# Performance work log

Measured on AMD Instinct MI355X. Metric: run time of the kernel, lower is better.

Reference implementation:

```python
import jax, jax.numpy as jnp
import numpy as np
import math

L, D, H, V, B, S, MR = 8, 768, 12, 32000, 2, 1024, 4
HD = D // H

def setup_inputs() -> dict:
    key = jax.random.key(0)
    ks = iter(jax.random.split(key, 64))
    def rn(shape, s=0.02):
        return jax.random.normal(next(ks), shape, jnp.float32) * s
    inp = {}
    inp['tokens'] = jax.random.randint(next(ks), (B, S), 0, V, jnp.int32)
    inp['tok_emb'] = rn((V, D))
    inp['pos_emb'] = rn((S, D))
    for n in ['Wq_row', 'Wk_row', 'Wv_row', 'Wq_col', 'Wo']:
        inp[n] = rn((L, D, D))
    for n in ['bq_row', 'bk_row', 'bv_row', 'bq_col', 'bo']:
        inp[n] = jnp.zeros((L, D), jnp.float32)
    inp['ln1_g'] = jnp.ones((L, D), jnp.float32); inp['ln1_b'] = jnp.zeros((L, D), jnp.float32)
    inp['ln2_g'] = jnp.ones((L, D), jnp.float32); inp['ln2_b'] = jnp.zeros((L, D), jnp.float32)
    inp['W1'] = rn((L, D, MR * D)); inp['b1'] = jnp.zeros((L, MR * D), jnp.float32)
    inp['W2'] = rn((L, MR * D, D)); inp['b2'] = jnp.zeros((L, D), jnp.float32)
    inp['Wk_sh'] = rn((D, D)); inp['bk_sh'] = jnp.zeros((D,), jnp.float32)
    inp['Wv_sh'] = rn((D, D)); inp['bv_sh'] = jnp.zeros((D,), jnp.float32)
    inp['lnf_g'] = jnp.ones((D,), jnp.float32); inp['lnf_b'] = jnp.zeros((D,), jnp.float32)
    inp['Whead'] = rn((D, V)); inp['bhead'] = jnp.zeros((V,), jnp.float32)
    return inp

def _ln(x, g, b, eps=1e-5):
    m = x.mean(-1, keepdims=True)
    v = ((x - m) ** 2).mean(-1, keepdims=True)
    return (x - m) * jax.lax.rsqrt(v + eps) * g + b

def _heads(x):
    b, s, _ = x.shape
    return x.reshape(b, s, H, HD).transpose(0, 2, 1, 3)  # [B,H,S,hd]

def _merge(x):
    b, h, s, hd = x.shape
    return x.transpose(0, 2, 1, 3).reshape(b, s, h * hd)

def _forward(tokens, tok_emb, pos_emb, Wq_row, bq_row, Wk_row, bk_row, Wv_row, bv_row,
             Wq_col, bq_col, Wo, bo, ln1_g, ln1_b, ln2_g, ln2_b, W1, b1, W2, b2,
             Wk_sh, bk_sh, Wv_sh, bv_sh, lnf_g, lnf_b, Whead, bhead):
    s_len = tokens.shape[1]
    inv = 1.0 / math.sqrt(HD)
    x = tok_emb[tokens] + pos_emb[:s_len]
    mask = jnp.triu(jnp.ones((s_len, s_len), bool), 1)
    past_k, past_v = [], []
    for i in range(L):
        h = _ln(x, ln1_g[i], ln1_b[i])
        q_row = _heads(h @ Wq_row[i] + bq_row[i])
        k_row = _heads(h @ Wk_row[i] + bk_row[i])
        v_row = _heads(h @ Wv_row[i] + bv_row[i])
        q_col = _heads(h @ Wq_col[i] + bq_col[i])
        k_col = _heads(h @ Wk_sh + bk_sh)   # shared KV projector (archived memory)
        v_col = _heads(h @ Wv_sh + bv_sh)
        ts = jnp.einsum('bhqd,bhkd->bhqk', q_row, k_row) * inv
        ts = jnp.where(mask, -jnp.inf, ts)
        if past_k:
            pk = jnp.stack(past_k, axis=3)  # [B,H,S,l,hd]
            pv = jnp.stack(past_v, axis=3)
            ms = jnp.einsum('bhsd,bhsld->bhsl', q_col, pk) * inv
            w = jax.nn.softmax(jnp.concatenate([ts, ms], axis=-1), axis=-1)
            tw, mw = w[..., :s_len], w[..., s_len:]
            ctx = (jnp.einsum('bhqk,bhkd->bhqd', tw, v_row)
                   + jnp.einsum('bhsl,bhsld->bhsd', mw, pv))
        else:
            ctx = jnp.einsum('bhqk,bhkd->bhqd', jax.nn.softmax(ts, axis=-1), v_row)
        x = x + (_merge(ctx) @ Wo[i] + bo[i])
        h2 = _ln(x, ln2_g[i], ln2_b[i])
        x = x + (jax.nn.gelu(h2 @ W1[i] + b1[i], approximate=False) @ W2[i] + b2[i])
        past_k.append(k_col)
        past_v.append(v_col)
    return _ln(x, lnf_g, lnf_b) @ Whead + bhead

def reference(tokens, tok_emb, pos_emb, Wq_row, bq_row, Wk_row, bk_row, Wv_row, bv_row,
              Wq_col, bq_col, Wo, bo, ln1_g, ln1_b, ln2_g, ln2_b, W1, b1, W2, b2,
              Wk_sh, bk_sh, Wv_sh, bv_sh, lnf_g, lnf_b, Whead, bhead):
    return _forward(tokens, tok_emb, pos_emb, Wq_row, bq_row, Wk_row, bk_row, Wv_row, bv_row,
                    Wq_col, bq_col, Wo, bo, ln1_g, ln1_b, ln2_g, ln2_b, W1, b1, W2, b2,
                    Wk_sh, bk_sh, Wv_sh, bv_sh, lnf_g, lnf_b, Whead, bhead)
```

## Files before the change

### kernel.cpp

```cpp
#include <hip/hip_runtime.h>
#include <hip/hip_bf16.h>
#include <math.h>

#define L_   8
#define D_   768
#define H_   12
#define V_   32000
#define B_   2
#define S_   1024
#define HD_  64
#define BS_  2048
#define DFF_ 3072

typedef __hip_bfloat16 bf16;
typedef __attribute__((ext_vector_type(8))) short bf16x8;
typedef __attribute__((ext_vector_type(4))) float f32x4;

#define CFUN(r) (((r) >> 1) & 3)

__device__ __forceinline__ void cp16(void* lds, const void* g) {
  __builtin_amdgcn_global_load_lds(
      (const __attribute__((address_space(1))) void*)g,
      (__attribute__((address_space(3))) void*)lds, 16, 0, 0);
}

__device__ __forceinline__ unsigned short f2bf(float v) {
  __hip_bfloat16 h = __float2bfloat16(v);
  return *reinterpret_cast<unsigned short*>(&h);
}
__device__ __forceinline__ float bf2f(unsigned short u) {
  return __uint_as_float(((unsigned)u) << 16);
}

__global__ __launch_bounds__(256) void k_embed(const int* __restrict__ tokens,
    const float* __restrict__ tok_emb, const float* __restrict__ pos_emb,
    float* __restrict__ x) {
  int idx = blockIdx.x * 256 + threadIdx.x;
  int row = idx / D_;
  int d   = idx - row * D_;
  int s   = row & (S_ - 1);
  int t   = tokens[row];
  x[idx] = tok_emb[(size_t)t * D_ + d] + pos_emb[(size_t)s * D_ + d];
}

__global__ __launch_bounds__(256) void k_ln(const float* __restrict__ x,
    const float* __restrict__ g, const float* __restrict__ b,
    bf16* __restrict__ out) {
  int row = blockIdx.x;
  const float* xr = x + (size_t)row * D_;
  int t = threadIdx.x;
  float v0 = xr[t], v1 = xr[t + 256], v2 = xr[t + 512];
  float s  = v0 + v1 + v2;
  float s2 = v0 * v0 + v1 * v1 + v2 * v2;
#pragma unroll
  for (int off = 32; off; off >>= 1) {
    s  += __shfl_down(s, off);
    s2 += __shfl_down(s2, off);
  }
  __shared__ float rs[4], rs2[4];
  __shared__ float mean_s, rstd_s;
  int wid = t >> 6;
  if ((t & 63) == 0) { rs[wid] = s; rs2[wid] = s2; }
  __syncthreads();
  if (t == 0) {
    float S1 = rs[0] + rs[1] + rs[2] + rs[3];
    float S2 = rs2[0] + rs2[1] + rs2[2] + rs2[3];
    float m  = S1 / D_;
    float var = S2 / D_ - m * m;
    mean_s = m;
    rstd_s = rsqrtf(var + 1e-5f);
  }
  __syncthreads();
  float m = mean_s, r = rstd_s;
  bf16* orow = out + (size_t)row * D_;
  orow[t]       = __float2bfloat16((v0 - m) * r * g[t]       + b[t]);
  orow[t + 256] = __float2bfloat16((v1 - m) * r * g[t + 256] + b[t + 256]);
  orow[t + 512] = __float2bfloat16((v2 - m) * r * g[t + 512] + b[t + 512]);
}

__global__ __launch_bounds__(256) void k_w2bf_t(const float* __restrict__ W,
    bf16* __restrict__ Wt, int K, int N, size_t ils, size_t ols) {
  __shared__ float t[32][33];
  const float* Wm = W + (size_t)blockIdx.z * ils;
  bf16* Wtm = Wt + (size_t)blockIdx.z * ols;
  int n0 = blockIdx.x * 32, k0 = blockIdx.y * 32;
  int tx = threadIdx.x;
  for (int i = threadIdx.y; i < 32; i += 8)
    t[i][tx] = Wm[(size_t)(k0 + i) * N + n0 + tx];
  __syncthreads();
  for (int i = threadIdx.y; i < 32; i += 8)
    Wtm[(size_t)(n0 + i) * K + k0 + tx] = __float2bfloat16(t[tx][i]);
}

__global__ __launch_bounds__(256) void k_bcat(const float* __restrict__ bq,
    const float* __restrict__ bk, const float* __restrict__ bqc,
    const float* __restrict__ bv, const float* __restrict__ bksh,
    const float* __restrict__ bvsh, float* __restrict__ b6) {
  int idx = blockIdx.x * 256 + threadIdx.x;
  if (idx >= L_ * 4608) return;
  int l = idx / 4608, c = idx - l * 4608;
  float v = (c < 768)  ? bq[l * 768 + c]
          : (c < 1536) ? bk[l * 768 + c - 768]
          : (c < 2304) ? bqc[l * 768 + c - 1536]
          : (c < 3072) ? bv[l * 768 + c - 2304]
          : (c < 3840) ? bksh[c - 3072]
                       : bvsh[c - 3840];
  b6[idx] = v;
}

__global__ __launch_bounds__(256) void k_red(float* __restrict__ x,
    const float* __restrict__ pk, const float* __restrict__ bias, int N) {
  const int i = (blockIdx.x * 256 + threadIdx.x) * 4;
  const int col = i % N;
  const size_t MN = (size_t)BS_ * N;
  float4 a  = *reinterpret_cast<const float4*>(x + i);
  float4 p0 = *reinterpret_cast<const float4*>(pk + i);
  float4 p1 = *reinterpret_cast<const float4*>(pk + MN + i);
  a.x += p0.x + p1.x + bias[col];
  a.y += p0.y + p1.y + bias[col + 1];
  a.z += p0.z + p1.z + bias[col + 2];
  a.w += p0.w + p1.w + bias[col + 3];
  *reinterpret_cast<float4*>(x + i) = a;
}

template <int BM, int EPI, int KSPL>
__global__ __launch_bounds__(256) void k_bgemm(
    const bf16* __restrict__ A, const bf16* __restrict__ Wt,
    const bf16* __restrict__ Wt2,
    const float* __restrict__ bias, const float* __restrict__ resid,
    float* __restrict__ Cf, bf16* __restrict__ Cb, bf16* __restrict__ Cb2,
    bf16* __restrict__ Cb3, int NM, int M, int N, int K) {
  constexpr int ASZ = BM * 64;
  constexpr int ALINES = BM / 64;
  constexpr int BSTRIDE = ASZ + 8192;
  constexpr int MF = BM / 32;
  __shared__ __align__(16) char smem[3 * BSTRIDE];
  const int tid = threadIdx.x;
  const int l = tid & 63, w = tid >> 6;
  const int wr = w >> 1, wc = w & 1;

  const int nwg = (int)gridDim.x;
  int id = (int)blockIdx.x;
  id = (id & 7) * (nwg >> 3) + (id >> 3);
  int sk = 0;
  if constexpr (KSPL == 2) {
    const int TT = nwg >> 1;
    sk = id / TT;
    id -= sk * TT;
  }
  const int m0 = (id % NM) * BM;
  const int n0 = (id / NM) * 128;
  const int kstart = sk * (K / KSPL);

  const int lane15 = l & 15, lg = l >> 4;

  const bf16* WB = Wt;
  int nb0 = n0;
  if constexpr (EPI == 6) {
    if (n0 >= 3072) { WB = Wt2; nb0 = n0 - 3072; }
  }

  const int r0 = tid >> 2, p0 = tid & 3;
  const char* aSrc[ALINES];
#pragma unroll
  for (int i = 0; i < ALINES; i++) {
    const int rr = i * 64 + r0;
    aSrc[i] = (const char*)(A + (size_t)(m0 + rr) * K + kstart) + ((p0 ^ CFUN(rr)) * 16);
  }
  const char* bSrc0 = (const char*)(WB + (size_t)(nb0 + r0) * K + kstart) + ((p0 ^ CFUN(r0)) * 16);
  const char* bSrc1 = (const char*)(WB + (size_t)(nb0 + 64 + r0) * K + kstart) + ((p0 ^ CFUN(64 + r0)) * 16);

  int aOff[MF], bOff[4];
#pragma unroll
  for (int mi = 0; mi < MF; mi++) {
    int r = wr * (BM / 2) + mi * 16 + lane15;
    aOff[mi] = r * 64 + ((lg ^ CFUN(r)) * 16);
  }
#pragma unroll
  for (int ni = 0; ni < 4; ni++) {
    int r = wc * 64 + ni * 16 + lane15;
    bOff[ni] = ASZ + r * 64 + ((lg ^ CFUN(r)) * 16);
  }

  f32x4 acc[MF][4];
#pragma unroll
  for (int mi = 0; mi < MF; mi++)
#pragma unroll
    for (int ni = 0; ni < 4; ni++) acc[mi][ni] = (f32x4){0.f, 0.f, 0.f, 0.f};

  auto stage = [&](int buf, int t) {
    const size_t kb = (size_t)t * 64;
    char* base = smem + buf * BSTRIDE;
#pragma unroll
    for (int i = 0; i < ALINES; i++)
      cp16(base + i * 4096 + w * 1024, aSrc[i] + kb);
    cp16(base + ASZ + w * 1024, bSrc0 + kb);
    cp16(base + ASZ + 4096 + w * 1024, bSrc1 + kb);
  };
  auto compute = [&](int buf) {
    const char* base = smem + buf * BSTRIDE;
    bf16x8 af[MF], bfr[4];
#pragma unroll
    for (int mi = 0; mi < MF; mi++) af[mi] = *(const bf16x8*)(base + aOff[mi]);
#pragma unroll
    for (int ni = 0; ni < 4; ni++) bfr[ni] = *(const bf16x8*)(base + bOff[ni]);
    __builtin_amdgcn_s_setprio(1);
#pragma unroll
    for (int mi = 0; mi < MF; mi++)
#pragma unroll
      for (int ni = 0; ni < 4; ni++)
        acc[mi][ni] = __builtin_amdgcn_mfma_f32_16x16x32_bf16(
            af[mi], bfr[ni], acc[mi][ni], 0, 0, 0);
    __builtin_amdgcn_s_setprio(0);
  };

  const int nk = (K / KSPL) >> 5;
  stage(0, 0);
  stage(1, 1);
  int buf = 0;
  for (int t = 0; t < nk; t++) {
    if (t + 1 < nk) {
      if constexpr (ALINES == 2) asm volatile("s_waitcnt vmcnt(4)" ::: "memory");
      else                       asm volatile("s_waitcnt vmcnt(3)" ::: "memory");
    } else {
      asm volatile("s_waitcnt vmcnt(0)" ::: "memory");
    }
    __builtin_amdgcn_s_barrier();
    if (t + 2 < nk) {
      int nb = buf + 2; if (nb >= 3) nb -= 3;
      stage(nb, t + 2);
    }
    compute(buf);
    buf = (buf == 2) ? 0 : buf + 1;
  }

#pragma unroll
  for (int ni = 0; ni < 4; ni++) {
    const int col = n0 + wc * 64 + ni * 16 + lane15;
    const float bv = bias[col];
#pragma unroll
    for (int mi = 0; mi < MF; mi++) {
      const int rowb = m0 + wr * (BM / 2) + mi * 16 + lg * 4;
      if constexpr (EPI == 6) {
        if (col < 2304) {
#pragma unroll
          for (int j = 0; j < 4; j++)
            Cb[(size_t)(rowb + j) * 2304 + col] = __float2bfloat16(acc[mi][ni][j] + bv);
        } else if (col < 3072) {
          ushort4 pk;
          pk.x = f2bf(acc[mi][ni][0] + bv);
          pk.y = f2bf(acc[mi][ni][1] + bv);
          pk.z = f2bf(acc[mi][ni][2] + bv);
          pk.w = f2bf(acc[mi][ni][3] + bv);
          const int bq = rowb >> 10, s = rowb & (S_ - 1);
          *reinterpret_cast<ushort4*>(
              (unsigned short*)Cb2 + ((size_t)(bq * 768 + (col - 2304))) * S_ + s) = pk;
        } else {
#pragma unroll
          for (int j = 0; j < 4; j++)
            Cb3[(size_t)(rowb + j) * 1536 + (col - 3072)] =
                __float2bfloat16(acc[mi][ni][j] + bv);
        }
      } else if constexpr (EPI == 7) {
#pragma unroll
        for (int j = 0; j < 4; j++)
          Cf[(size_t)sk * M * N + (size_t)(rowb + j) * N + col] = acc[mi][ni][j];
      } else {
#pragma unroll
        for (int j = 0; j < 4; j++) {
          const int row = rowb + j;
          float v = acc[mi][ni][j] + bv;
          if constexpr (EPI == 1) v += resid[(size_t)row * N + col];
          if constexpr (EPI == 2) {
            v = 0.5f * v * (1.0f + erff(v * 0.70710678118654752f));
            Cb[(size_t)row * N + col] = __float2bfloat16(v);
          } else if constexpr (EPI == 3) {
            Cb[(size_t)row * N + col] = __float2bfloat16(v);
          } else {
            Cf[(size_t)row * N + col] = v;
          }
        }
      }
    }
  }
}

#define HBAR() asm volatile("s_barrier" ::: "memory")
#define MFMA16(AF, BF, MB, NB)                                               \
  do {                                                                       \
    __builtin_amdgcn_s_setprio(1);                                           \
    _Pragma("unroll") for (int mi_ = 0; mi_ < 4; mi_++)                      \
      _Pragma("unroll") for (int ni_ = 0; ni_ < 2; ni_++)                    \
        _Pragma("unroll") for (int ks_ = 0; ks_ < 2; ks_++)                  \
          acc[(MB) + mi_][(NB) + ni_] =                                      \
              __builtin_amdgcn_mfma_f32_16x16x32_bf16(                       \
                  AF[mi_][ks_], BF[ni_][ks_], acc[(MB) + mi_][(NB) + ni_],   \
                  0, 0, 0);                                                  \
    __builtin_amdgcn_s_setprio(0);                                           \
  } while (0)

__global__ __launch_bounds__(512, 1) void k_head8(const bf16* __restrict__ A,
    const bf16* __restrict__ Wt, const float* __restrict__ bias,
    float* __restrict__ C) {
  __shared__ __align__(16) char smem[131072];
  const int tid = threadIdx.x;
  const int l = tid & 63, w = tid >> 6;
  const int wr = w >> 2, wc = w & 3;
  const int lane15 = l & 15, lg = l >> 4;

  int id = (int)blockIdx.x;
  id = (id & 7) * 125 + (id >> 3);
  const int m0 = (id % 8) * 256;
  const int n0 = (id / 8) * 256;

  auto issueA = [&](int tile, int hb) {
#pragma unroll
    for (int j = 0; j < 2; j++) {
      const int idx = j * 512 + tid;
      const int rl = idx >> 3, sl = idx & 7;
      const bf16* g = A + (size_t)(m0 + hb + rl) * 768 + tile * 64 +
                      ((sl ^ (rl & 7)) << 3);
      cp16(smem + (tile & 1) * 32768 + hb * 128 + (j * 512 + w * 64) * 16, g);
    }
  };
  auto issueB = [&](int tile, int hb) {
#pragma unroll
    for (int j = 0; j < 2; j++) {
      const int idx = j * 512 + tid;
      const int rl = idx >> 3, sl = idx & 7;
      const bf16* g = Wt + (size_t)(n0 + hb + rl) * 768 + tile * 64 +
                      ((sl ^ (rl & 7)) << 3);
      cp16(smem + 65536 + (tile & 1) * 32768 + hb * 128 + (j * 512 + w * 64) * 16, g);
    }
  };
  auto ldA = [&](int buf, int mi, int ks) {
    const int r = wr * 128 + mi * 16 + lane15;
    return *(const bf16x8*)(smem + buf * 32768 + r * 128 +
                            ((((ks << 2) + lg) ^ (r & 7)) << 4));
  };
  auto ldB = [&](int buf, int ni, int ks) {
    const int r = wc * 64 + ni * 16 + lane15;
    return *(const bf16x8*)(smem + 65536 + buf * 32768 + r * 128 +
                            ((((ks << 2) + lg) ^ (r & 7)) << 4));
  };

  f32x4 acc[8][4];
#pragma unroll
  for (int i = 0; i < 8; i++)
#pragma unroll
    for (int j = 0; j < 4; j++) acc[i][j] = (f32x4){0.f, 0.f, 0.f, 0.f};
  bf16x8 alo[4][2], ahi[4][2], blo[2][2], bhi[2][2];

  issueA(0, 0);  issueA(0, 128);  issueB(0, 0);  issueB(0, 128);
  issueB(1, 0);  issueA(1, 0);    issueB(1, 128);
  asm volatile("s_waitcnt vmcnt(6)" ::: "memory");
  HBAR();

  for (int it = 0; it < 5; ++it) {
    const int Tb = 2 * it + 1, Tn = 2 * it + 2;
#pragma unroll
    for (int mi = 0; mi < 4; mi++) { alo[mi][0] = ldA(0, mi, 0); alo[mi][1] = ldA(0, mi, 1); }
#pragma unroll
    for (int ni = 0; ni < 2; ni++) { blo[ni][0] = ldB(0, ni, 0); blo[ni][1] = ldB(0, ni, 1); }
    issueA(Tb, 128);
    HBAR(); MFMA16(alo, blo, 0, 0); HBAR();
#pragma unroll
    for (int ni = 0; ni < 2; ni++) { bhi[ni][0] = ldB(0, ni + 2, 0); bhi[ni][1] = ldB(0, ni + 2, 1); }
    HBAR(); MFMA16(alo, bhi, 0, 2); HBAR();
#pragma unroll
    for (int mi = 0; mi < 4; mi++) { ahi[mi][0] = ldA(0, mi + 4, 0); ahi[mi][1] = ldA(0, mi + 4, 1); }
    issueB(Tn, 0);
    HBAR(); MFMA16(ahi, bhi, 4, 2); HBAR();
    issueA(Tn, 0);
    issueB(Tn, 128);
    asm volatile("s_waitcnt vmcnt(6)" ::: "memory");
    HBAR(); MFMA16(ahi, blo, 4, 0); HBAR();
#pragma unroll
    for (int mi = 0; mi < 4; mi++) { alo[mi][0] = ldA(1, mi, 0); alo[mi][1] = ldA(1, mi, 1); }
#pragma unroll
    for (int ni = 0; ni < 2; ni++) { blo[ni][0] = ldB(1, ni, 0); blo[ni][1] = ldB(1, ni, 1); }
    issueA(Tn, 128);
    HBAR(); MFMA16(alo, blo, 0, 0); HBAR();
#pragma unroll
    for (int ni = 0; ni < 2; ni++) { bhi[ni][0] = ldB(1, ni + 2, 0); bhi[ni][1] = ldB(1, ni + 2, 1); }
    HBAR(); MFMA16(alo, bhi, 0, 2); HBAR();
#pragma unroll
    for (int mi = 0; mi < 4; mi++) { ahi[mi][0] = ldA(1, mi + 4, 0); ahi[mi][1] = ldA(1, mi + 4, 1); }
    issueB(Tn + 1, 0);
    HBAR(); MFMA16(ahi, bhi, 4, 2); HBAR();
    issueA(Tn + 1, 0);
    issueB(Tn + 1, 128);
    asm volatile("s_waitcnt vmcnt(6)" ::: "memory");
    HBAR(); MFMA16(ahi, blo, 4, 0); HBAR();
  }

  {
#pragma unroll
    for (int mi = 0; mi < 4; mi++) { alo[mi][0] = ldA(0, mi, 0); alo[mi][1] = ldA(0, mi, 1); }
#pragma unroll
    for (int ni = 0; ni < 2; ni++) { blo[ni][0] = ldB(0, ni, 0); blo[ni][1] = ldB(0, ni, 1); }
    issueA(11, 128);
    HBAR(); MFMA16(alo, blo, 0, 0); HBAR();
#pragma unroll
    for (int ni = 0; ni < 2; ni++) { bhi[ni][0] = ldB(0, ni + 2, 0); bhi[ni][1] = ldB(0, ni + 2, 1); }
    HBAR(); MFMA16(alo, bhi, 0, 2); HBAR();
#pragma unroll
    for (int mi = 0; mi < 4; mi++) { ahi[mi][0] = ldA(0, mi + 4, 0); ahi[mi][1] = ldA(0, mi + 4, 1); }
    HBAR(); MFMA16(ahi, bhi, 4, 2); HBAR();
    asm volatile("s_waitcnt vmcnt(0)" ::: "memory");
    HBAR(); MFMA16(ahi, blo, 4, 0); HBAR();
#pragma unroll
    for (int mi = 0; mi < 4; mi++) { alo[mi][0] = ldA(1, mi, 0); alo[mi][1] = ldA(1, mi, 1); }
#pragma unroll
    for (int ni = 0; ni < 2; ni++) { blo[ni][0] = ldB(1, ni, 0); blo[ni][1] = ldB(1, ni, 1); }
    MFMA16(alo, blo, 0, 0);
#pragma unroll
    for (int ni = 0; ni < 2; ni++) { bhi[ni][0] = ldB(1, ni + 2, 0); bhi[ni][1] = ldB(1, ni + 2, 1); }
    MFMA16(alo, bhi, 0, 2);
#pragma unroll
    for (int mi = 0; mi < 4; mi++) { ahi[mi][0] = ldA(1, mi + 4, 0); ahi[mi][1] = ldA(1, mi + 4, 1); }
    MFMA16(ahi, bhi, 4, 2);
    MFMA16(ahi, blo, 4, 0);
  }

#pragma unroll
  for (int ni = 0; ni < 4; ni++) {
    const int col = n0 + wc * 64 + ni * 16 + lane15;
    const float bv = bias[col];
#pragma unroll
    for (int mi = 0; mi < 8; mi++) {
      const int rowb = m0 + wr * 128 + mi * 16 + lg * 4;
#pragma unroll
      for (int j = 0; j < 4; j++)
        C[(size_t)(rowb + j) * 32000 + col] = acc[mi][ni][j] + bv;
    }
  }
}

__global__ __launch_bounds__(256) void k_attn(
    const bf16* __restrict__ qkv, const bf16* __restrict__ vT,
    const bf16* __restrict__ memkv, bf16* __restrict__ ctx, int layer) {
  const int bh = blockIdx.x;
  const int b = bh / H_, h = bh % H_;
  const int qt = (int)gridDim.y - 1 - (int)blockIdx.y;
  const int tid = threadIdx.x;
  const int w = tid >> 6, l = tid & 63;
  const int lane15 = l & 15, lg = l >> 4;
  const float inv = 0.125f;

  __shared__ char plds[4][2048];
  __shared__ float wlp[4][16][16];
  char* pl = plds[w];

  const int qrow0 = qt * 64 + w * 16;
  const size_t rowA = (size_t)(b * S_ + qrow0 + lane15);
  const bf16* qp = qkv + rowA * 2304 + h * 64 + lg * 8;
  const bf16x8 qf0 = *(const bf16x8*)(qp);
  const bf16x8 qf1 = *(const bf16x8*)(qp + 32);

  const bf16* kbase = qkv + (size_t)(b * S_) * 2304 + 768 + h * 64 + lg * 8;
  const bf16* vbase = vT + ((size_t)(b * 768 + h * 64 + lane15)) * S_;

  float mrow[4], dsum[4];
  f32x4 acc[4];
#pragma unroll
  for (int j = 0; j < 4; j++) { mrow[j] = -INFINITY; dsum[j] = 0.f; }
#pragma unroll
  for (int ni = 0; ni < 4; ni++) acc[ni] = (f32x4){0.f, 0.f, 0.f, 0.f};

  const int ntile = ((qrow0 + 15) >> 6) + 1;
  for (int kt64 = 0; kt64 < ntile; kt64++) {
    const int k0 = kt64 * 64;
    f32x4 sc[4];
#pragma unroll
    for (int kt = 0; kt < 4; kt++) {
      const bf16* kp = kbase + (size_t)(k0 + kt * 16 + lane15) * 2304;
      bf16x8 kf0 = *(const bf16x8*)(kp);
      bf16x8 kf1 = *(const bf16x8*)(kp + 32);
      f32x4 z = (f32x4){0.f, 0.f, 0.f, 0.f};
      z = __builtin_amdgcn_mfma_f32_16x16x32_bf16(qf0, kf0, z, 0, 0, 0);
      sc[kt] = __builtin_amdgcn_mfma_f32_16x16x32_bf16(qf1, kf1, z, 0, 0, 0);
    }
    float tmax[4];
#pragma unroll
    for (int j = 0; j < 4; j++) tmax[j] = -INFINITY;
#pragma unroll
    for (int kt = 0; kt < 4; kt++) {
      const int kabs = k0 + kt * 16 + lane15;
#pragma unroll
      for (int j = 0; j < 4; j++) {
        const int qabs = qrow0 + lg * 4 + j;
        float v = (kabs <= qabs) ? sc[kt][j] * inv : -INFINITY;
        sc[kt][j] = v;
        tmax[j] = fmaxf(tmax[j], v);
      }
    }
#pragma unroll
    for (int off = 1; off < 16; off <<= 1)
#pragma unroll
      for (int j = 0; j < 4; j++) tmax[j] = fmaxf(tmax[j], __shfl_xor(tmax[j], off, 16));

    float psum[4];
#pragma unroll
    for (int j = 0; j < 4; j++) {
      const float mnew = fmaxf(mrow[j], tmax[j]);
      const float alpha = __expf(mrow[j] - mnew);
      mrow[j] = mnew;
      dsum[j] *= alpha;
#pragma unroll
      for (int ni = 0; ni < 4; ni++) acc[ni][j] *= alpha;
      psum[j] = 0.f;
    }
#pragma unroll
    for (int kt = 0; kt < 4; kt++) {
      const int gsl = kt * 2 + (lane15 >> 3);
      const int ebyte = (lane15 & 7) * 2;
#pragma unroll
      for (int j = 0; j < 4; j++) {
        const float p = __expf(sc[kt][j] - mrow[j]);
        psum[j] += p;
        const int r = lg * 4 + j;
        *(unsigned short*)(pl + r * 128 + ((gsl ^ (r & 7)) << 4) + ebyte) = f2bf(p);
      }
    }
#pragma unroll
    for (int off = 1; off < 16; off <<= 1)
#pragma unroll
      for (int j = 0; j < 4; j++) psum[j] += __shfl_xor(psum[j], off, 16);
#pragma unroll
    for (int j = 0; j < 4; j++) dsum[j] += psum[j];

#pragma unroll
    for (int ks = 0; ks < 2; ks++) {
      bf16x8 pa = *(const bf16x8*)(pl + lane15 * 128 +
                                   ((((ks << 2) + lg) ^ (lane15 & 7)) << 4));
      const bf16* vp = vbase + k0 + ks * 32 + lg * 8;
#pragma unroll
      for (int ni = 0; ni < 4; ni++) {
        bf16x8 vf = *(const bf16x8*)(vp + (size_t)ni * 16 * S_);
        acc[ni] = __builtin_amdgcn_mfma_f32_16x16x32_bf16(pa, vf, acc[ni], 0, 0, 0);
      }
    }
  }

  const int r4 = lg * 4;
  if (lane15 < layer) {
    const int ml = lane15;
#pragma unroll
    for (int j = 0; j < 4; j++) {
      const size_t rowB = (size_t)(b * S_) + qrow0 + r4 + j;
      const bf16* qc = qkv + rowB * 2304 + 1536 + h * 64;
      const bf16* mk = memkv + ((size_t)ml * BS_ + rowB) * 1536 + h * 64;
      float d_ = 0.f;
#pragma unroll
      for (int t = 0; t < 8; t++) {
        bf16x8 qv = *(const bf16x8*)(qc + t * 8);
        bf16x8 kv = *(const bf16x8*)(mk + t * 8);
#pragma unroll
        for (int e = 0; e < 8; e++)
          d_ += bf2f((unsigned short)qv[e]) * bf2f((unsigned short)kv[e]);
      }
      wlp[w][r4 + j][ml] = d_ * inv;
    }
  }
  if (layer > 0) {
#pragma unroll
    for (int j = 0; j < 4; j++) {
      const int r = r4 + j;
      float mm = -INFINITY;
      for (int ml = 0; ml < layer; ml++) mm = fmaxf(mm, wlp[w][r][ml]);
      const float mnew = fmaxf(mrow[j], mm);
      const float alpha = __expf(mrow[j] - mnew);
      mrow[j] = mnew;
      dsum[j] *= alpha;
#pragma unroll
      for (int ni = 0; ni < 4; ni++) acc[ni][j] *= alpha;
      const size_t rowB = (size_t)(b * S_) + qrow0 + r;
      for (int ml = 0; ml < layer; ml++) {
        const float p = __expf(wlp[w][r][ml] - mnew);
        dsum[j] += p;
        const unsigned short* mv = (const unsigned short*)(memkv +
            ((size_t)ml * BS_ + rowB) * 1536 + 768 + h * 64 + lane15);
#pragma unroll
        for (int ni = 0; ni < 4; ni++)
          acc[ni][j] += p * bf2f(mv[ni * 16]);
      }
    }
  }

#pragma unroll
  for (int j = 0; j < 4; j++) {
    const float rd = 1.f / dsum[j];
    const size_t rowB = (size_t)(b * S_) + qrow0 + r4 + j;
    bf16* cp = ctx + rowB * 768 + h * 64 + lane15;
#pragma unroll
    for (int ni = 0; ni < 4; ni++)
      cp[ni * 16] = __float2bfloat16(acc[ni][j] * rd);
  }
}

extern "C" void kernel_launch(void* const* d_in, const int* in_sizes, int n_in,
                              void* d_out, int out_size, void* d_ws, size_t ws_size,
                              hipStream_t stream) {
  const int*   tokens  = (const int*)d_in[0];
  const float* tok_emb = (const float*)d_in[1];
  const float* pos_emb = (const float*)d_in[2];
  const float *Wq_row, *Wk_row, *Wv_row, *Wq_col, *Wo;
  const float *bq_row, *bk_row, *bv_row, *bq_col, *bo;
  if (in_sizes[4] == L_ * D_ * D_) {
    Wq_row = (const float*)d_in[3];  Wk_row = (const float*)d_in[4];
    Wv_row = (const float*)d_in[5];  Wq_col = (const float*)d_in[6];
    Wo     = (const float*)d_in[7];
    bq_row = (const float*)d_in[8];  bk_row = (const float*)d_in[9];
    bv_row = (const float*)d_in[10]; bq_col = (const float*)d_in[11];
    bo     = (const float*)d_in[12];
  } else {
    Wq_row = (const float*)d_in[3];  bq_row = (const float*)d_in[4];
    Wk_row = (const float*)d_in[5];  bk_row = (const float*)d_in[6];
    Wv_row = (const float*)d_in[7];  bv_row = (const float*)d_in[8];
    Wq_col = (const float*)d_in[9];  bq_col = (const float*)d_in[10];
    Wo     = (const float*)d_in[11]; bo     = (const float*)d_in[12];
  }
  const float* ln1_g = (const float*)d_in[13]; const float* ln1_b = (const float*)d_in[14];
  const float* ln2_g = (const float*)d_in[15]; const float* ln2_b = (const float*)d_in[16];
  const float* W1    = (const float*)d_in[17]; const float* b1    = (const float*)d_in[18];
  const float* W2    = (const float*)d_in[19]; const float* b2    = (const float*)d_in[20];
  const float* Wk_sh = (const float*)d_in[21]; const float* bk_sh = (const float*)d_in[22];
  const float* Wv_sh = (const float*)d_in[23]; const float* bv_sh = (const float*)d_in[24];
  const float* lnf_g = (const float*)d_in[25]; const float* lnf_b = (const float*)d_in[26];
  const float* Whead = (const float*)d_in[27]; const float* bhead = (const float*)d_in[28];

  char* p = (char*)d_ws;
  float* x      = (float*)p; p += (size_t)BS_ * D_ * 4;
  bf16*  h_bf   = (bf16*)p;  p += (size_t)BS_ * D_ * 2;
  bf16*  qkv3   = (bf16*)p;  p += (size_t)BS_ * 2304 * 2;
  bf16*  vTb    = (bf16*)p;  p += (size_t)B_ * 768 * S_ * 2;
  bf16*  memkv  = (bf16*)p;  p += (size_t)L_ * BS_ * 1536 * 2;
  bf16*  ctx_bf = (bf16*)p;  p += (size_t)BS_ * D_ * 2;
  bf16*  mlp_bf = (bf16*)p;  p += (size_t)BS_ * DFF_ * 2;
  float* pkbuf  = (float*)p; p += (size_t)2 * BS_ * D_ * 4;
  float* b6cat  = (float*)p; p += (size_t)L_ * 4608 * 4;
  bf16* tW6    = (bf16*)p; p += (size_t)L_ * 3072 * D_ * 2;
  bf16* tWsh   = (bf16*)p; p += (size_t)1536 * D_ * 2;
  bf16* tWo    = (bf16*)p; p += (size_t)L_ * D_ * D_ * 2;
  bf16* tW1    = (bf16*)p; p += (size_t)L_ * DFF_ * D_ * 2;
  bf16* tW2    = (bf16*)p; p += (size_t)L_ * D_ * DFF_ * 2;
  bf16* tWhead = (bf16*)p; p += (size_t)V_ * D_ * 2;

  dim3 tb(32, 8);
  const size_t DD = (size_t)D_ * D_;
  const size_t W6S = (size_t)3072 * 768;
  k_w2bf_t<<<dim3(24, 24, L_), tb, 0, stream>>>(Wq_row, tW6,              768, 768, DD, W6S);
  k_w2bf_t<<<dim3(24, 24, L_), tb, 0, stream>>>(Wk_row, tW6 + 768 * 768,  768, 768, DD, W6S);
  k_w2bf_t<<<dim3(24, 24, L_), tb, 0, stream>>>(Wq_col, tW6 + 1536 * 768, 768, 768, DD, W6S);
  k_w2bf_t<<<dim3(24, 24, L_), tb, 0, stream>>>(Wv_row, tW6 + 2304 * 768, 768, 768, DD, W6S);
  k_w2bf_t<<<dim3(24, 24, 1), tb, 0, stream>>>(Wk_sh, tWsh,             768, 768, 0, 0);
  k_w2bf_t<<<dim3(24, 24, 1), tb, 0, stream>>>(Wv_sh, tWsh + 768 * 768, 768, 768, 0, 0);
  k_w2bf_t<<<dim3(24, 24, L_), tb, 0, stream>>>(Wo,     tWo, 768, 768, DD, DD);
  k_w2bf_t<<<dim3(96, 24, L_), tb, 0, stream>>>(W1, tW1, 768, 3072, (size_t)768 * 3072, (size_t)3072 * 768);
  k_w2bf_t<<<dim3(24, 96, L_), tb, 0, stream>>>(W2, tW2, 3072, 768, (size_t)768 * 3072, (size_t)768 * 3072);
  k_w2bf_t<<<dim3(1000, 24, 1), tb, 0, stream>>>(Whead, tWhead, 768, 32000, 0, 0);
  k_bcat<<<dim3(144), 256, 0, stream>>>(bq_row, bk_row, bq_col, bv_row, bk_sh, bv_sh, b6cat);

  k_embed<<<dim3((BS_ * D_) / 256), 256, 0, stream>>>(tokens, tok_emb, pos_emb, x);

  for (int i = 0; i < L_; i++) {
    k_ln<<<dim3(BS_), 256, 0, stream>>>(x, ln1_g + i * D_, ln1_b + i * D_, h_bf);
    k_bgemm<128, 6, 1><<<dim3(576), 256, 0, stream>>>(
        h_bf, tW6 + (size_t)i * W6S, tWsh, b6cat + (size_t)i * 4608,
        nullptr, nullptr, qkv3, vTb, memkv + (size_t)i * BS_ * 1536,
        16, BS_, 4608, 768);
    k_attn<<<dim3(B_ * H_, S_ / 64), 256, 0, stream>>>(qkv3, vTb, memkv, ctx_bf, i);
    k_bgemm<64, 1, 1><<<dim3(192), 256, 0, stream>>>(
        ctx_bf, tWo + (size_t)i * DD, nullptr, bo + i * D_, x, x,
        nullptr, nullptr, nullptr, 32, BS_, 768, 768);
    k_ln<<<dim3(BS_), 256, 0, stream>>>(x, ln2_g + i * D_, ln2_b + i * D_, h_bf);
    k_bgemm<128, 2, 1><<<dim3(384), 256, 0, stream>>>(
        h_bf, tW1 + (size_t)i * 3072 * 768, nullptr, b1 + (size_t)i * DFF_,
        nullptr, nullptr, mlp_bf, nullptr, nullptr, 16, BS_, 3072, 768);
    k_bgemm<64, 7, 2><<<dim3(384), 256, 0, stream>>>(
        mlp_bf, tW2 + (size_t)i * 768 * 3072, nullptr, b2 + i * D_,
        nullptr, pkbuf, nullptr, nullptr, nullptr, 32, BS_, 768, 3072);
    k_red<<<dim3((BS_ * D_) / 1024), 256, 0, stream>>>(x, pkbuf, b2 + i * D_, D_);
  }
  k_ln<<<dim3(BS_), 256, 0, stream>>>(x, lnf_g, lnf_b, h_bf);
  k_head8<<<dim3(1000), 512, 0, stream>>>(h_bf, tWhead, bhead, (float*)d_out);
}
```

Baseline: 1.772 ms.

## Fuse split-K reduction with next LayerNorm and streamline attention softmax

```diff
diff --git a/kernel.cpp b/kernel.cpp
--- a/kernel.cpp
+++ b/kernel.cpp
@@ -73,6 +73,50 @@
   __syncthreads();
   float m = mean_s, r = rstd_s;
   bf16* orow = out + (size_t)row * D_;
+  orow[t]       = __float2bfloat16((v0 - m) * r * g[t]       + b[t]);
+  orow[t + 256] = __float2bfloat16((v1 - m) * r * g[t + 256] + b[t + 256]);
+  orow[t + 512] = __float2bfloat16((v2 - m) * r * g[t + 512] + b[t + 512]);
+}
+
+__global__ __launch_bounds__(256) void k_redln(float* __restrict__ x,
+    const float* __restrict__ pk, const float* __restrict__ b2,
+    const float* __restrict__ g, const float* __restrict__ b,
+    bf16* __restrict__ out) {
+  const int row = blockIdx.x;
+  const int t = threadIdx.x;
+  const size_t base = (size_t)row * D_;
+  const size_t MN = (size_t)BS_ * D_;
+  float v0, v1, v2;
+  {
+    int c0 = t, c1 = t + 256, c2 = t + 512;
+    v0 = x[base + c0] + pk[base + c0] + pk[MN + base + c0] + b2[c0];
+    v1 = x[base + c1] + pk[base + c1] + pk[MN + base + c1] + b2[c1];
+    v2 = x[base + c2] + pk[base + c2] + pk[MN + base + c2] + b2[c2];
+    x[base + c0] = v0; x[base + c1] = v1; x[base + c2] = v2;
+  }
+  float s  = v0 + v1 + v2;
+  float s2 = v0 * v0 + v1 * v1 + v2 * v2;
+#pragma unroll
+  for (int off = 32; off; off >>= 1) {
+    s  += __shfl_down(s, off);
+    s2 += __shfl_down(s2, off);
+  }
+  __shared__ float rs[4], rs2[4];
+  __shared__ float mean_s, rstd_s;
+  int wid = t >> 6;
+  if ((t & 63) == 0) { rs[wid] = s; rs2[wid] = s2; }
+  __syncthreads();
+  if (t == 0) {
+    float S1 = rs[0] + rs[1] + rs[2] + rs[3];
+    float S2 = rs2[0] + rs2[1] + rs2[2] + rs2[3];
+    float m  = S1 / D_;
+    float var = S2 / D_ - m * m;
+    mean_s = m;
+    rstd_s = rsqrtf(var + 1e-5f);
+  }
+  __syncthreads();
+  float m = mean_s, r = rstd_s;
+  bf16* orow = out + base;
   orow[t]       = __float2bfloat16((v0 - m) * r * g[t]       + b[t]);
   orow[t + 256] = __float2bfloat16((v1 - m) * r * g[t + 256] + b[t + 256]);
   orow[t + 512] = __float2bfloat16((v2 - m) * r * g[t + 512] + b[t + 512]);
@@ -106,21 +150,6 @@
           : (c < 3840) ? bksh[c - 3072]
                        : bvsh[c - 3840];
   b6[idx] = v;
-}
-
-__global__ __launch_bounds__(256) void k_red(float* __restrict__ x,
-    const float* __restrict__ pk, const float* __restrict__ bias, int N) {
-  const int i = (blockIdx.x * 256 + threadIdx.x) * 4;
-  const int col = i % N;
-  const size_t MN = (size_t)BS_ * N;
-  float4 a  = *reinterpret_cast<const float4*>(x + i);
-  float4 p0 = *reinterpret_cast<const float4*>(pk + i);
-  float4 p1 = *reinterpret_cast<const float4*>(pk + MN + i);
-  a.x += p0.x + p1.x + bias[col];
-  a.y += p0.y + p1.y + bias[col + 1];
-  a.z += p0.z + p1.z + bias[col + 2];
-  a.w += p0.w + p1.w + bias[col + 3];
-  *reinterpret_cast<float4*>(x + i) = a;
 }
 
 template <int BM, int EPI, int KSPL>
@@ -455,8 +484,15 @@
   const int qrow0 = qt * 64 + w * 16;
   const size_t rowA = (size_t)(b * S_ + qrow0 + lane15);
   const bf16* qp = qkv + rowA * 2304 + h * 64 + lg * 8;
-  const bf16x8 qf0 = *(const bf16x8*)(qp);
-  const bf16x8 qf1 = *(const bf16x8*)(qp + 32);
+  auto scale8 = [](bf16x8 v) {
+    bf16x8 r;
+#pragma unroll
+    for (int e = 0; e < 8; e++)
+      r[e] = (short)f2bf(bf2f((unsigned short)v[e]) * 0.125f);
+    return r;
+  };
+  const bf16x8 qf0 = scale8(*(const bf16x8*)(qp));
+  const bf16x8 qf1 = scale8(*(const bf16x8*)(qp + 32));
 
   const bf16* kbase = qkv + (size_t)(b * S_) * 2304 + 768 + h * 64 + lg * 8;
   const bf16* vbase = vT + ((size_t)(b * 768 + h * 64 + lane15)) * S_;
@@ -484,33 +520,45 @@
     float tmax[4];
 #pragma unroll
     for (int j = 0; j < 4; j++) tmax[j] = -INFINITY;
-#pragma unroll
-    for (int kt = 0; kt < 4; kt++) {
-      const int kabs = k0 + kt * 16 + lane15;
+    const bool needMask = (k0 + 63 > qrow0);
+    if (needMask) {
+#pragma unroll
+      for (int kt = 0; kt < 4; kt++) {
+        const int kabs = k0 + kt * 16 + lane15;
+#pragma unroll
+        for (int j = 0; j < 4; j++) {
+          const int qabs = qrow0 + lg * 4 + j;
+          float v = (kabs <= qabs) ? sc[kt][j] : -INFINITY;
+          sc[kt][j] = v;
+          tmax[j] = fmaxf(tmax[j], v);
+        }
+      }
+    } else {
+#pragma unroll
+      for (int kt = 0; kt < 4; kt++)
+#pragma unroll
+        for (int j = 0; j < 4; j++) tmax[j] = fmaxf(tmax[j], sc[kt][j]);
+    }
+#pragma unroll
+    for (int off = 1; off < 16; off <<= 1)
+#pragma unroll
+      for (int j = 0; j < 4; j++) tmax[j] = fmaxf(tmax[j], __shfl_xor(tmax[j], off, 16));
+
+    bool grow = false;
+#pragma unroll
+    for (int j = 0; j < 4; j++) grow |= (tmax[j] > mrow[j]);
+    if (__ballot(grow) != 0ull) {
 #pragma unroll
       for (int j = 0; j < 4; j++) {
-        const int qabs = qrow0 + lg * 4 + j;
-        float v = (kabs <= qabs) ? sc[kt][j] * inv : -INFINITY;
-        sc[kt][j] = v;
-        tmax[j] = fmaxf(tmax[j], v);
+        const float mnew = fmaxf(mrow[j], tmax[j]);
+        const float alpha = __expf(mrow[j] - mnew);
+        mrow[j] = mnew;
+        dsum[j] *= alpha;
+#pragma unroll
+        for (int ni = 0; ni < 4; ni++) acc[ni][j] *= alpha;
       }
     }
-#pragma unroll
-    for (int off = 1; off < 16; off <<= 1)
-#pragma unroll
-      for (int j = 0; j < 4; j++) tmax[j] = fmaxf(tmax[j], __shfl_xor(tmax[j], off, 16));
-
-    float psum[4];
-#pragma unroll
-    for (int j = 0; j < 4; j++) {
-      const float mnew = fmaxf(mrow[j], tmax[j]);
-      const float alpha = __expf(mrow[j] - mnew);
-      mrow[j] = mnew;
-      dsum[j] *= alpha;
-#pragma unroll
-      for (int ni = 0; ni < 4; ni++) acc[ni][j] *= alpha;
-      psum[j] = 0.f;
-    }
+    float psum[4] = {0.f, 0.f, 0.f, 0.f};
 #pragma unroll
     for (int kt = 0; kt < 4; kt++) {
       const int gsl = kt * 2 + (lane15 >> 3);
@@ -663,9 +711,9 @@
   k_bcat<<<dim3(144), 256, 0, stream>>>(bq_row, bk_row, bq_col, bv_row, bk_sh, bv_sh, b6cat);
 
   k_embed<<<dim3((BS_ * D_) / 256), 256, 0, stream>>>(tokens, tok_emb, pos_emb, x);
+  k_ln<<<dim3(BS_), 256, 0, stream>>>(x, ln1_g, ln1_b, h_bf);
 
   for (int i = 0; i < L_; i++) {
-    k_ln<<<dim3(BS_), 256, 0, stream>>>(x, ln1_g + i * D_, ln1_b + i * D_, h_bf);
     k_bgemm<128, 6, 1><<<dim3(576), 256, 0, stream>>>(
         h_bf, tW6 + (size_t)i * W6S, tWsh, b6cat + (size_t)i * 4608,
         nullptr, nullptr, qkv3, vTb, memkv + (size_t)i * BS_ * 1536,
@@ -681,8 +729,9 @@
     k_bgemm<64, 7, 2><<<dim3(384), 256, 0, stream>>>(
         mlp_bf, tW2 + (size_t)i * 768 * 3072, nullptr, b2 + i * D_,
         nullptr, pkbuf, nullptr, nullptr, nullptr, 32, BS_, 768, 3072);
-    k_red<<<dim3((BS_ * D_) / 1024), 256, 0, stream>>>(x, pkbuf, b2 + i * D_, D_);
-  }
-  k_ln<<<dim3(BS_), 256, 0, stream>>>(x, lnf_g, lnf_b, h_bf);
+    const float* gn = (i < L_ - 1) ? (ln1_g + (i + 1) * D_) : lnf_g;
+    const float* bn = (i < L_ - 1) ? (ln1_b + (i + 1) * D_) : lnf_b;
+    k_redln<<<dim3(BS_), 256, 0, stream>>>(x, pkbuf, b2 + i * D_, gn, bn, h_bf);
+  }
   k_head8<<<dim3(1000), 512, 0, stream>>>(h_bf, tWhead, bhead, (float*)d_out);
 }
```

Measured after the change: 1.638 ms. 1.08x faster.
